# Optimization experiments

Measured on AMD Instinct MI355X. Metric: run time of the kernel, lower is better.

## Reference

```python
import jax, jax.numpy as jnp
import numpy as np
from jax import lax

C = 64          # grid_channels
RGB = 3         # rgb_channels
D = 128         # conditioning_dim
NUM_CLASSES = 1000
HIDDEN = 256    # hypernet hidden
NUM_STEPS = 32
TOT1 = C * C * 9


def setup_inputs() -> dict:
    key = jax.random.key(0)
    ks = jax.random.split(key, 20)
    s = 0.02
    B, H, W = 32, 64, 64
    return {
        "class_labels": jax.random.randint(ks[0], (B,), 0, NUM_CLASSES),
        "initial_grid": jax.random.normal(ks[1], (B, C, H, W), jnp.float32) * 0.1,
        "emb": jax.random.normal(ks[2], (NUM_CLASSES, D), jnp.float32) * s,
        "hw1": jax.random.normal(ks[3], (D, HIDDEN), jnp.float32) * s,
        "hb1": jnp.zeros((HIDDEN,), jnp.float32),
        "hw2": jax.random.normal(ks[4], (HIDDEN, HIDDEN), jnp.float32) * s,
        "hb2": jnp.zeros((HIDDEN,), jnp.float32),
        "hw3": jax.random.normal(ks[5], (HIDDEN, 2 * TOT1), jnp.float32) * s,
        "hb3": jnp.zeros((2 * TOT1,), jnp.float32),
        "f1w1": jax.random.normal(ks[6], (D, D), jnp.float32) * s,
        "f1b1": jnp.zeros((D,), jnp.float32),
        "f1w2": jax.random.normal(ks[7], (D, 2 * C), jnp.float32) * s,
        "f1b2": jnp.concatenate([jnp.ones((C,), jnp.float32), jnp.zeros((C,), jnp.float32)]),
        "f2w1": jax.random.normal(ks[8], (D, D), jnp.float32) * s,
        "f2b1": jnp.zeros((D,), jnp.float32),
        "f2w2": jax.random.normal(ks[9], (D, 2 * C), jnp.float32) * s,
        "f2b2": jnp.concatenate([jnp.ones((C,), jnp.float32), jnp.zeros((C,), jnp.float32)]),
        "blend": jnp.float32(0.5),
    }


def _conv_circ_one(x, w):
    # x: [C,H,W], w: [Cout,Cin,3,3]; circular pad then VALID conv == padding=1 circular
    xp = jnp.pad(x, ((0, 0), (1, 1), (1, 1)), mode='wrap')
    return lax.conv_general_dilated(xp[None], w, (1, 1), 'VALID')[0]

_bconv = jax.vmap(_conv_circ_one)  # per-sample dynamic weights over batch


def _film_params(cond, w1, b1, w2, b2):
    p = jax.nn.relu(cond @ w1 + b1) @ w2 + b2  # [B, 2C]
    return p[:, :C, None, None], p[:, C:, None, None]


def reference(class_labels, initial_grid, emb, hw1, hb1, hw2, hb2, hw3, hb3,
              f1w1, f1b1, f1w2, f1b2, f2w1, f2b1, f2w2, f2b2, blend):
    cond = emb[class_labels]                       # [B, D]
    h = jax.nn.relu(cond @ hw1 + hb1)
    h = jax.nn.relu(h @ hw2 + hb2)
    weights = h @ hw3 + hb3                        # [B, 2*C*C*9]
    B = cond.shape[0]
    w1 = weights[:, :TOT1].reshape(B, C, C, 3, 3)
    w2 = weights[:, TOT1:].reshape(B, C, C, 3, 3)
    g1, be1 = _film_params(cond, f1w1, f1b1, f1w2, f1b2)
    g2, be2 = _film_params(cond, f2w1, f2b1, f2w2, f2b2)
    blend_s = jax.nn.sigmoid(blend)

    def step(grid, _):
        u = jax.nn.relu(g1 * _bconv(grid, w1) + be1)
        u = jax.nn.relu(g2 * _bconv(u, w2) + be2)
        grid = (1 - blend_s) * grid + blend_s * u
        rgb = jax.nn.sigmoid(grid[:, :RGB])
        return grid, rgb

    _, traj = lax.scan(step, initial_grid, None, length=NUM_STEPS)  # [T,B,3,H,W]
    return traj[-1], traj
```

## Files before the change

kernel.cpp:

```cpp
#include <hip/hip_runtime.h>


typedef __attribute__((ext_vector_type(8))) short short8;
typedef __attribute__((ext_vector_type(4))) float f32x4;
typedef __attribute__((ext_vector_type(8))) unsigned short us8;

__device__ __forceinline__ unsigned short f2bf(float f) {
  unsigned int u = __builtin_bit_cast(unsigned int, f);
  u = (u + 0x7FFFu + ((u >> 16) & 1u)) >> 16;
  return (unsigned short)u;
}
__device__ __forceinline__ float bf2f(unsigned short h) {
  unsigned int u = ((unsigned int)h) << 16;
  return __builtin_bit_cast(float, u);
}

__device__ __forceinline__ void gl_lds16(const void* g, void* l) {
  __builtin_amdgcn_global_load_lds((const __attribute__((address_space(1))) void*)g,
                                   (__attribute__((address_space(3))) void*)l, 16, 0, 0);
}

__global__ void hyper_kernel(const int* __restrict__ labels, const float* __restrict__ emb,
                             const float* __restrict__ hw1, const float* __restrict__ hb1,
                             const float* __restrict__ hw2, const float* __restrict__ hb2,
                             float* __restrict__ h2T) {
  __shared__ float cond[128];
  __shared__ float h1[256];
  const int s = blockIdx.x, j = threadIdx.x;
  if (j < 128) cond[j] = emb[(size_t)labels[s] * 128 + j];
  __syncthreads();
  float a = hb1[j];
  for (int k = 0; k < 128; ++k) a += cond[k] * hw1[k * 256 + j];
  h1[j] = fmaxf(a, 0.f);
  __syncthreads();
  float a2 = hb2[j];
  for (int k = 0; k < 256; ++k) a2 += h1[k] * hw2[k * 256 + j];
  h2T[j * 32 + s] = fmaxf(a2, 0.f);
}

__global__ void film_kernel(const int* __restrict__ labels, const float* __restrict__ emb,
                            const float* __restrict__ f1w1, const float* __restrict__ f1b1,
                            const float* __restrict__ f1w2, const float* __restrict__ f1b2,
                            const float* __restrict__ f2w1, const float* __restrict__ f2b1,
                            const float* __restrict__ f2w2, const float* __restrict__ f2b2,
                            float* __restrict__ film) {
  __shared__ float cond[128];
  __shared__ float hid[128];
  const int s = blockIdx.x, which = blockIdx.y, j = threadIdx.x;
  const float* W1 = which ? f2w1 : f1w1;
  const float* B1 = which ? f2b1 : f1b1;
  const float* W2 = which ? f2w2 : f1w2;
  const float* B2 = which ? f2b2 : f1b2;
  cond[j] = emb[(size_t)labels[s] * 128 + j];
  __syncthreads();
  float a = B1[j];
  for (int k = 0; k < 128; ++k) a += cond[k] * W1[k * 128 + j];
  hid[j] = fmaxf(a, 0.f);
  __syncthreads();
  float p = B2[j];
  for (int k = 0; k < 128; ++k) p += hid[k] * W2[k * 128 + j];
  film[(size_t)((which * 2 + (j >> 6)) * 32 + s) * 64 + (j & 63)] = p;
}

__launch_bounds__(256)
__global__ void wgen_kernel(const float* __restrict__ h2T, const float* __restrict__ hw3,
                            const float* __restrict__ hb3, unsigned short* __restrict__ W) {
  __shared__ float h2l[8192];
  const int t = threadIdx.x;
  for (int i = t; i < 8192; i += 256) h2l[i] = h2T[i];
  __syncthreads();
  const int lane = t & 63, sg = t >> 6;
  const int j0 = blockIdx.x * 128 + lane * 2;
  const float* __restrict__ gp = hw3 + j0;
  const float* __restrict__ hp = h2l + sg * 8;

  float acc[16];
  #pragma unroll
  for (int i = 0; i < 16; ++i) acc[i] = 0.f;

  float2 bA[8], bB[8], bC[8], bD[8];
  #pragma unroll
  for (int u = 0; u < 8; ++u) bA[u] = *(const float2*)(gp + (size_t)(u) * 73728);
  #pragma unroll
  for (int u = 0; u < 8; ++u) bB[u] = *(const float2*)(gp + (size_t)(8 + u) * 73728);
  #pragma unroll
  for (int u = 0; u < 8; ++u) bC[u] = *(const float2*)(gp + (size_t)(16 + u) * 73728);

#define WG_COMPUTE(BUF, KB)                                                    \
  _Pragma("unroll")                                                            \
  for (int u = 0; u < 8; ++u) {                                                \
    const float4 hA = *(const float4*)(hp + ((KB) + u) * 32);                  \
    const float4 hB = *(const float4*)(hp + ((KB) + u) * 32 + 4);              \
    const float2 wv = BUF[u];                                                  \
    acc[0]  += hA.x * wv.x; acc[1]  += hA.x * wv.y;                            \
    acc[2]  += hA.y * wv.x; acc[3]  += hA.y * wv.y;                            \
    acc[4]  += hA.z * wv.x; acc[5]  += hA.z * wv.y;                            \
    acc[6]  += hA.w * wv.x; acc[7]  += hA.w * wv.y;                            \
    acc[8]  += hB.x * wv.x; acc[9]  += hB.x * wv.y;                            \
    acc[10] += hB.y * wv.x; acc[11] += hB.y * wv.y;                            \
    acc[12] += hB.z * wv.x; acc[13] += hB.z * wv.y;                            \
    acc[14] += hB.w * wv.x; acc[15] += hB.w * wv.y;                            \
  }

  #pragma unroll 1
  for (int kc = 0; kc < 256; kc += 32) {
    #pragma unroll
    for (int u = 0; u < 8; ++u) bD[u] = *(const float2*)(gp + (size_t)(kc + 24 + u) * 73728);
    WG_COMPUTE(bA, kc)
    if (kc < 224) {
      #pragma unroll
      for (int u = 0; u < 8; ++u) bA[u] = *(const float2*)(gp + (size_t)(kc + 32 + u) * 73728);
    }
    WG_COMPUTE(bB, kc + 8)
    if (kc < 224) {
      #pragma unroll
      for (int u = 0; u < 8; ++u) bB[u] = *(const float2*)(gp + (size_t)(kc + 40 + u) * 73728);
    }
    WG_COMPUTE(bC, kc + 16)
    if (kc < 224) {
      #pragma unroll
      for (int u = 0; u < 8; ++u) bC[u] = *(const float2*)(gp + (size_t)(kc + 48 + u) * 73728);
    }
    WG_COMPUTE(bD, kc + 24)
  }
#undef WG_COMPUTE

  #pragma unroll
  for (int c = 0; c < 2; ++c) {
    const int j  = j0 + c;
    const float bias = hb3[j];
    const int cv = j / 36864;
    const int r  = j - cv * 36864;
    const int co = r / 576;
    const int r2 = r - co * 576;
    const int ci = r2 / 9;
    const int tap = r2 - ci * 9;
    const int sw = (co * 64 + ci) ^ ((co & 7) << 3);
    #pragma unroll
    for (int i = 0; i < 8; ++i) {
      const int s2 = sg * 8 + i;
      W[(size_t)((s2 * 2 + cv) * 9 + tap) * 4096 + sw] = f2bf(acc[i * 2 + c] + bias);
    }
  }
}

__global__ void init_kernel(const float* __restrict__ gin, unsigned short* __restrict__ g0) {
  __shared__ float lds[64][65];
  const int b = blockIdx.x >> 6, y = blockIdx.x & 63;
  const int t = threadIdx.x;
  {
    const int ci = t >> 2, xq = t & 3;
    const float* base = gin + (size_t)((b * 64 + ci) * 64 + y) * 64;
    #pragma unroll
    for (int q = 0; q < 4; ++q) {
      const int x0 = (xq + q * 4) * 4;
      const float4 v = *(const float4*)(base + x0);
      lds[ci][x0+0] = v.x; lds[ci][x0+1] = v.y; lds[ci][x0+2] = v.z; lds[ci][x0+3] = v.w;
    }
  }
  __syncthreads();
  const int x = t >> 2, cq = t & 3, ci0 = cq * 16;
  us8 lo, hi;
  #pragma unroll
  for (int i = 0; i < 8; ++i) lo[i] = f2bf(lds[ci0 + i][x]);
  #pragma unroll
  for (int i = 0; i < 8; ++i) hi[i] = f2bf(lds[ci0 + 8 + i][x]);
  char* dbase = (char*)(g0 + (size_t)(b * 64 + y) * 4096);
  const int o = x * 128 + ci0 * 2, sw = (x & 7) << 4;
  *(us8*)(dbase + (o ^ sw)) = lo;
  *(us8*)(dbase + ((o + 16) ^ sw)) = hi;
}

template<int WHICH>
__launch_bounds__(512, 2)
__global__ void conv_kernel(const unsigned short* __restrict__ Wall,
                            const unsigned short* __restrict__ src,
                            unsigned short* __restrict__ dst,
                            const unsigned short* __restrict__ gold,
                            const float* __restrict__ film,
                            const float* __restrict__ blendp,
                            float* __restrict__ out, int t) {
  __shared__ unsigned short in_lds[10 * 4096];
  __shared__ unsigned short w_lds[9 * 4096];
  const int tid  = threadIdx.x;
  const int wid  = tid >> 6;
  const int lane = tid & 63;
  const int l15  = lane & 15;
  const int lhi  = lane >> 4;
  const int b    = blockIdx.x;
  const int s    = (b & 7) + 8 * ((b >> 3) & 3);
  const int y0   = (b >> 5) * 8;

  const unsigned short* srcs = src + (size_t)s * 262144;
  const unsigned short* Wb   = Wall + (size_t)((s * 2 + WHICH) * 9) * 4096;

  #pragma unroll
  for (int q = 0; q < 10; ++q) {
    const int c   = q * 8 + wid;
    const int row = c >> 3, part = c & 7;
    const int gy  = (y0 + row + 63) & 63;
    gl_lds16(srcs + gy * 4096 + part * 512 + lane * 8, &in_lds[row * 4096 + part * 512]);
  }
  #pragma unroll
  for (int q = 0; q < 9; ++q) {
    const int c = q * 8 + wid;
    gl_lds16(Wb + c * 512 + lane * 8, &w_lds[c * 512]);
  }
  asm volatile("s_waitcnt vmcnt(0)" ::: "memory");
  __syncthreads();

  f32x4 acc[4][4];
  #pragma unroll
  for (int m = 0; m < 4; ++m)
    #pragma unroll
    for (int n = 0; n < 4; ++n)
      #pragma unroll
      for (int j = 0; j < 4; ++j) acc[m][n][j] = 0.f;

  short8 afA[4][2], bfA[4][2], afB[4][2], bfB[4][2];

#define CONV_LOAD(AF, BF, TAP)                                                  \
  {                                                                             \
    const int ky = (TAP) / 3, kx = (TAP) % 3;                                   \
    _Pragma("unroll")                                                           \
    for (int m = 0; m < 4; ++m) {                                               \
      const int co = m * 16 + l15;                                              \
      _Pragma("unroll")                                                         \
      for (int kk = 0; kk < 2; ++kk) {                                          \
        const int off = (TAP) * 8192 +                                          \
            ((co * 128 + kk * 64 + lhi * 16) ^ ((co & 7) << 4));                \
        AF[m][kk] = *(const short8*)((const char*)w_lds + off);                 \
      }                                                                         \
    }                                                                           \
    const int r = wid + ky;                                                     \
    _Pragma("unroll")                                                           \
    for (int n = 0; n < 4; ++n) {                                               \
      const int xs = (n * 16 + l15 + kx + 63) & 63;                             \
      _Pragma("unroll")                                                         \
      for (int kk = 0; kk < 2; ++kk) {                                          \
        const int off = r * 8192 +                                              \
            ((xs * 128 + kk * 64 + lhi * 16) ^ ((xs & 7) << 4));                \
        BF[n][kk] = *(const short8*)((const char*)in_lds + off);                \
      }                                                                         \
    }                                                                           \
  }

#define CONV_MMAC(AF, BF)                                                       \
  __builtin_amdgcn_s_setprio(1);                                                \
  _Pragma("unroll")                                                             \
  for (int kk = 0; kk < 2; ++kk)                                                \
    _Pragma("unroll")                                                           \
    for (int m = 0; m < 4; ++m)                                                 \
      _Pragma("unroll")                                                         \
      for (int n = 0; n < 4; ++n)                                               \
        acc[m][n] = __builtin_amdgcn_mfma_f32_16x16x32_bf16(                    \
            AF[m][kk], BF[n][kk], acc[m][n], 0, 0, 0);                          \
  __builtin_amdgcn_s_setprio(0);

  CONV_LOAD(afA, bfA, 0)
  CONV_LOAD(afB, bfB, 1)  CONV_MMAC(afA, bfA)
  CONV_LOAD(afA, bfA, 2)  CONV_MMAC(afB, bfB)
  CONV_LOAD(afB, bfB, 3)  CONV_MMAC(afA, bfA)
  CONV_LOAD(afA, bfA, 4)  CONV_MMAC(afB, bfB)
  CONV_LOAD(afB, bfB, 5)  CONV_MMAC(afA, bfA)
  CONV_LOAD(afA, bfA, 6)  CONV_MMAC(afB, bfB)
  CONV_LOAD(afB, bfB, 7)  CONV_MMAC(afA, bfA)
  CONV_LOAD(afA, bfA, 8)  CONV_MMAC(afB, bfB)
  CONV_MMAC(afA, bfA)
#undef CONV_LOAD
#undef CONV_MMAC

  const int y = y0 + wid;
  const float* fg = film + WHICH * 2 * 2048;
  const float* fb = fg + 2048;
  float bs = 0.f, obs = 0.f;
  if (WHICH == 1) { bs = 1.f / (1.f + expf(-blendp[0])); obs = 1.f - bs; }
  unsigned short* drow = dst + (size_t)s * 262144 + y * 4096;
  const unsigned short* grow = (WHICH == 1) ? (gold + (size_t)s * 262144 + y * 4096) : (const unsigned short*)nullptr;

  #pragma unroll
  for (int m = 0; m < 4; ++m) {
    const int co0 = m * 16 + lhi * 4;
    const float4 g  = *(const float4*)&fg[s * 64 + co0];
    const float4 be = *(const float4*)&fb[s * 64 + co0];
    #pragma unroll
    for (int n = 0; n < 4; ++n) {
      const int x = n * 16 + l15;
      const int off = (x * 128 + co0 * 2) ^ ((x & 7) << 4);
      const f32x4 v = acc[m][n];
      const float u0 = fmaxf(g.x * v[0] + be.x, 0.f);
      const float u1 = fmaxf(g.y * v[1] + be.y, 0.f);
      const float u2 = fmaxf(g.z * v[2] + be.z, 0.f);
      const float u3 = fmaxf(g.w * v[3] + be.w, 0.f);
      if (WHICH == 0) {
        ushort4 pk; pk.x = f2bf(u0); pk.y = f2bf(u1); pk.z = f2bf(u2); pk.w = f2bf(u3);
        *(ushort4*)((char*)drow + off) = pk;
      } else {
        const ushort4 od = *(const ushort4*)((const char*)grow + off);
        const float g0 = obs * bf2f(od.x) + bs * u0;
        const float g1 = obs * bf2f(od.y) + bs * u1;
        const float g2 = obs * bf2f(od.z) + bs * u2;
        const float g3 = obs * bf2f(od.w) + bs * u3;
        ushort4 pk; pk.x = f2bf(g0); pk.y = f2bf(g1); pk.z = f2bf(g2); pk.w = f2bf(g3);
        *(ushort4*)((char*)drow + off) = pk;
        if (co0 == 0) {
          const float r0 = 1.f / (1.f + expf(-g0));
          const float r1 = 1.f / (1.f + expf(-g1));
          const float r2 = 1.f / (1.f + expf(-g2));
          float* ob = out + 393216 + (size_t)((t * 32 + s) * 3) * 4096 + y * 64 + x;
          ob[0] = r0; ob[4096] = r1; ob[8192] = r2;
          if (t == 31) {
            float* o2 = out + (size_t)(s * 3) * 4096 + y * 64 + x;
            o2[0] = r0; o2[4096] = r1; o2[8192] = r2;
          }
        }
      }
    }
  }
}

extern "C" void kernel_launch(void* const* d_in, const int* in_sizes, int n_in,
                              void* d_out, int out_size, void* d_ws, size_t ws_size,
                              hipStream_t stream) {
  (void)in_sizes; (void)n_in; (void)out_size; (void)ws_size;
  const int*   labels = (const int*)d_in[0];
  const float* gin    = (const float*)d_in[1];
  const float* emb    = (const float*)d_in[2];
  const float* hw1    = (const float*)d_in[3];
  const float* hb1    = (const float*)d_in[4];
  const float* hw2    = (const float*)d_in[5];
  const float* hb2    = (const float*)d_in[6];
  const float* hw3    = (const float*)d_in[7];
  const float* hb3    = (const float*)d_in[8];
  const float* f1w1   = (const float*)d_in[9];
  const float* f1b1   = (const float*)d_in[10];
  const float* f1w2   = (const float*)d_in[11];
  const float* f1b2   = (const float*)d_in[12];
  const float* f2w1   = (const float*)d_in[13];
  const float* f2b1   = (const float*)d_in[14];
  const float* f2w2   = (const float*)d_in[15];
  const float* f2b2   = (const float*)d_in[16];
  const float* blend  = (const float*)d_in[17];
  float* out = (float*)d_out;

  char* ws = (char*)d_ws;
  unsigned short* grid0 = (unsigned short*)(ws + (size_t)0);
  unsigned short* grid1 = (unsigned short*)(ws + (size_t)16777216);
  unsigned short* ubuf  = (unsigned short*)(ws + (size_t)33554432);
  unsigned short* Wbuf  = (unsigned short*)(ws + (size_t)50331648);
  float* h2T  = (float*)(ws + (size_t)55050240);
  float* film = (float*)(ws + (size_t)55083008);

  hyper_kernel<<<32, 256, 0, stream>>>(labels, emb, hw1, hb1, hw2, hb2, h2T);
  film_kernel<<<dim3(32, 2), 128, 0, stream>>>(labels, emb, f1w1, f1b1, f1w2, f1b2,
                                               f2w1, f2b1, f2w2, f2b2, film);
  wgen_kernel<<<576, 256, 0, stream>>>(h2T, hw3, hb3, Wbuf);
  init_kernel<<<2048, 256, 0, stream>>>(gin, grid0);

  for (int t = 0; t < 32; ++t) {
    unsigned short* gi = (t & 1) ? grid1 : grid0;
    unsigned short* go = (t & 1) ? grid0 : grid1;
    conv_kernel<0><<<256, 512, 0, stream>>>(Wbuf, gi, ubuf, nullptr, film, nullptr, nullptr, t);
    conv_kernel<1><<<256, 512, 0, stream>>>(Wbuf, ubuf, go, gi, film, blend, out, t);
  }
}
```

Baseline: 1.234 ms.

## Stage hypernet weight tiles through LDS with async double-buffered global_load_lds

The weight-generation GEMM now streams hw3 tiles of 32 rows by 128 columns into a double-buffered LDS array using direct global-to-LDS loads, instead of each thread keeping four register buffers of float2 loads. The thread mapping changes to one column per thread with 16 samples per thread group, and the output stores change to match. The intent is to cut register pressure and get wider, better-coalesced loads from the large hw3 matrix. The cost is extra LDS use and a barrier per k-chunk.

```diff
diff --git a/kernel.cpp b/kernel.cpp
--- a/kernel.cpp
+++ b/kernel.cpp
@@ -66,81 +66,67 @@
 __global__ void wgen_kernel(const float* __restrict__ h2T, const float* __restrict__ hw3,
                             const float* __restrict__ hb3, unsigned short* __restrict__ W) {
   __shared__ float h2l[8192];
+  __shared__ float wbuf[2][32 * 128];
   const int t = threadIdx.x;
   for (int i = t; i < 8192; i += 256) h2l[i] = h2T[i];
-  __syncthreads();
-  const int lane = t & 63, sg = t >> 6;
-  const int j0 = blockIdx.x * 128 + lane * 2;
-  const float* __restrict__ gp = hw3 + j0;
-  const float* __restrict__ hp = h2l + sg * 8;
+  const int lane = t & 63, wid = t >> 6;
+  const int col = t & 127;
+  const int sg  = t >> 7;
+  const int j   = blockIdx.x * 128 + col;
+  const float* __restrict__ hp = h2l + sg * 16;
+
+  const int i0   = (lane >> 5);
+  const int csub = (lane & 31) << 2;
+#define WG_STAGE(BUF, KC)                                                      \
+  _Pragma("unroll")                                                            \
+  for (int q = 0; q < 4; ++q) {                                                \
+    const int ii = q * 4 + wid;                                                \
+    gl_lds16(hw3 + (size_t)((KC) + 2 * ii + i0) * 73728 + blockIdx.x * 128 + csub, \
+             &wbuf[BUF][2 * ii * 128]);                                        \
+  }
 
   float acc[16];
   #pragma unroll
   for (int i = 0; i < 16; ++i) acc[i] = 0.f;
 
-  float2 bA[8], bB[8], bC[8], bD[8];
-  #pragma unroll
-  for (int u = 0; u < 8; ++u) bA[u] = *(const float2*)(gp + (size_t)(u) * 73728);
-  #pragma unroll
-  for (int u = 0; u < 8; ++u) bB[u] = *(const float2*)(gp + (size_t)(8 + u) * 73728);
-  #pragma unroll
-  for (int u = 0; u < 8; ++u) bC[u] = *(const float2*)(gp + (size_t)(16 + u) * 73728);
-
-#define WG_COMPUTE(BUF, KB)                                                    \
-  _Pragma("unroll")                                                            \
-  for (int u = 0; u < 8; ++u) {                                                \
-    const float4 hA = *(const float4*)(hp + ((KB) + u) * 32);                  \
-    const float4 hB = *(const float4*)(hp + ((KB) + u) * 32 + 4);              \
-    const float2 wv = BUF[u];                                                  \
-    acc[0]  += hA.x * wv.x; acc[1]  += hA.x * wv.y;                            \
-    acc[2]  += hA.y * wv.x; acc[3]  += hA.y * wv.y;                            \
-    acc[4]  += hA.z * wv.x; acc[5]  += hA.z * wv.y;                            \
-    acc[6]  += hA.w * wv.x; acc[7]  += hA.w * wv.y;                            \
-    acc[8]  += hB.x * wv.x; acc[9]  += hB.x * wv.y;                            \
-    acc[10] += hB.y * wv.x; acc[11] += hB.y * wv.y;                            \
-    acc[12] += hB.z * wv.x; acc[13] += hB.z * wv.y;                            \
-    acc[14] += hB.w * wv.x; acc[15] += hB.w * wv.y;                            \
-  }
-
+  WG_STAGE(0, 0)
+  asm volatile("s_waitcnt vmcnt(0)" ::: "memory");
+  __syncthreads();
+
+  int buf = 0;
   #pragma unroll 1
   for (int kc = 0; kc < 256; kc += 32) {
+    if (kc + 32 < 256) WG_STAGE(buf ^ 1, kc + 32)
     #pragma unroll
-    for (int u = 0; u < 8; ++u) bD[u] = *(const float2*)(gp + (size_t)(kc + 24 + u) * 73728);
-    WG_COMPUTE(bA, kc)
-    if (kc < 224) {
-      #pragma unroll
-      for (int u = 0; u < 8; ++u) bA[u] = *(const float2*)(gp + (size_t)(kc + 32 + u) * 73728);
+    for (int kk = 0; kk < 32; ++kk) {
+      const float wv = wbuf[buf][kk * 128 + col];
+      const float4 hA = *(const float4*)(hp + (kc + kk) * 32);
+      const float4 hB = *(const float4*)(hp + (kc + kk) * 32 + 4);
+      const float4 hC = *(const float4*)(hp + (kc + kk) * 32 + 8);
+      const float4 hD = *(const float4*)(hp + (kc + kk) * 32 + 12);
+      acc[0]  += hA.x * wv; acc[1]  += hA.y * wv; acc[2]  += hA.z * wv; acc[3]  += hA.w * wv;
+      acc[4]  += hB.x * wv; acc[5]  += hB.y * wv; acc[6]  += hB.z * wv; acc[7]  += hB.w * wv;
+      acc[8]  += hC.x * wv; acc[9]  += hC.y * wv; acc[10] += hC.z * wv; acc[11] += hC.w * wv;
+      acc[12] += hD.x * wv; acc[13] += hD.y * wv; acc[14] += hD.z * wv; acc[15] += hD.w * wv;
     }
-    WG_COMPUTE(bB, kc + 8)
-    if (kc < 224) {
-      #pragma unroll
-      for (int u = 0; u < 8; ++u) bB[u] = *(const float2*)(gp + (size_t)(kc + 40 + u) * 73728);
-    }
-    WG_COMPUTE(bC, kc + 16)
-    if (kc < 224) {
-      #pragma unroll
-      for (int u = 0; u < 8; ++u) bC[u] = *(const float2*)(gp + (size_t)(kc + 48 + u) * 73728);
-    }
-    WG_COMPUTE(bD, kc + 24)
-  }
-#undef WG_COMPUTE
-
-  #pragma unroll
-  for (int c = 0; c < 2; ++c) {
-    const int j  = j0 + c;
-    const float bias = hb3[j];
-    const int cv = j / 36864;
-    const int r  = j - cv * 36864;
-    const int co = r / 576;
-    const int r2 = r - co * 576;
-    const int ci = r2 / 9;
-    const int tap = r2 - ci * 9;
-    const int sw = (co * 64 + ci) ^ ((co & 7) << 3);
-    #pragma unroll
-    for (int i = 0; i < 8; ++i) {
-      const int s2 = sg * 8 + i;
-      W[(size_t)((s2 * 2 + cv) * 9 + tap) * 4096 + sw] = f2bf(acc[i * 2 + c] + bias);
-    }
+    asm volatile("s_waitcnt vmcnt(0)" ::: "memory");
+    __syncthreads();
+    buf ^= 1;
+  }
+#undef WG_STAGE
+
+  const float bias = hb3[j];
+  const int cv = j / 36864;
+  const int r  = j - cv * 36864;
+  const int co = r / 576;
+  const int r2 = r - co * 576;
+  const int ci = r2 / 9;
+  const int tap = r2 - ci * 9;
+  const int sw = (co * 64 + ci) ^ ((co & 7) << 3);
+  #pragma unroll
+  for (int i = 0; i < 16; ++i) {
+    const int s2 = sg * 16 + i;
+    W[(size_t)((s2 * 2 + cv) * 9 + tap) * 4096 + sw] = f2bf(acc[i] + bias);
   }
 }
 
```

Result: no change. 1.217 ms (-1.4%).
